# Kernel tuning notes

Measured on AMD Instinct MI355X. Metric: run time of the kernel, lower is better.

## Reference

```python
import jax, jax.numpy as jnp
import numpy as np

DIM = 2048
NH = 16
HD = DIM // NH
B = 2
S = 2048
HID = 5632  # multiple_of*ceil(int(2*4*dim/3)/multiple_of)
EPS = 1e-6


def setup_inputs() -> dict:
    key = jax.random.key(0)
    ks = jax.random.split(key, 9)
    sd = 0.02
    x = jax.random.normal(ks[0], (B, S, DIM), jnp.float32)
    wq = jax.random.normal(ks[1], (DIM, DIM), jnp.float32) * sd
    wk = jax.random.normal(ks[2], (DIM, DIM), jnp.float32) * sd
    wv = jax.random.normal(ks[3], (DIM, DIM), jnp.float32) * sd
    wo = jax.random.normal(ks[4], (DIM, DIM), jnp.float32) * sd
    w1 = jax.random.normal(ks[5], (DIM, HID), jnp.float32) * sd
    w2 = jax.random.normal(ks[6], (HID, DIM), jnp.float32) * sd
    w3 = jax.random.normal(ks[7], (DIM, HID), jnp.float32) * sd
    attn_norm_w = jnp.ones((DIM,), jnp.float32)
    ffn_norm_w = jnp.ones((DIM,), jnp.float32)
    # RoPE tables: freqs_cis = exp(i * t * theta_j), theta_j = 10000^(-2j/HD)
    inv_freq = 1.0 / (10000.0 ** (np.arange(0, HD, 2).astype(np.float32) / HD))
    t = np.arange(S, dtype=np.float32)
    ang = np.outer(t, inv_freq)  # [S, HD/2]
    freqs_cos = jnp.asarray(np.cos(ang), jnp.float32)
    freqs_sin = jnp.asarray(np.sin(ang), jnp.float32)
    # causal additive mask [1,1,S,S]
    mask = jnp.triu(jnp.full((S, S), float('-inf'), jnp.float32), k=1)[None, None]
    return dict(x=x, wq=wq, wk=wk, wv=wv, wo=wo, w1=w1, w2=w2, w3=w3,
                attn_norm_w=attn_norm_w, ffn_norm_w=ffn_norm_w,
                freqs_cos=freqs_cos, freqs_sin=freqs_sin, mask=mask)


def _rmsnorm(x, w):
    xf = x.astype(jnp.float32)
    v = jnp.mean(xf * xf, axis=-1, keepdims=True)
    return (xf * jax.lax.rsqrt(v + EPS)).astype(x.dtype) * w


def _rope(t, cos, sin):
    # t: [B,S,H,HD] -> pairs (re, im) on last dim
    tr = t.reshape(*t.shape[:-1], HD // 2, 2)
    re, im = tr[..., 0], tr[..., 1]
    c = cos[None, :, None, :]
    s = sin[None, :, None, :]
    out_re = re * c - im * s
    out_im = re * s + im * c
    return jnp.stack([out_re, out_im], axis=-1).reshape(t.shape)


def reference(x, wq, wk, wv, wo, w1, w2, w3, attn_norm_w, ffn_norm_w,
              freqs_cos, freqs_sin, mask):
    # --- attention sublayer ---
    h_in = _rmsnorm(x, attn_norm_w)
    xq = (h_in @ wq).reshape(B, S, NH, HD)
    xk = (h_in @ wk).reshape(B, S, NH, HD)
    xv = (h_in @ wv).reshape(B, S, NH, HD)
    xq = _rope(xq, freqs_cos, freqs_sin)
    xk = _rope(xk, freqs_cos, freqs_sin)
    scale = 1.0 / jnp.sqrt(jnp.float32(HD))
    scores = jnp.einsum('bqhd,bkhd->bhqk', xq, xk) * scale + mask
    probs = jax.nn.softmax(scores.astype(jnp.float32), axis=-1).astype(xq.dtype)
    attn = jnp.einsum('bhqk,bkhd->bqhd', probs, xv).reshape(B, S, DIM)
    h = x + attn @ wo
    # --- feedforward sublayer (SwiGLU) ---
    f_in = _rmsnorm(h, ffn_norm_w)
    ffn = (jax.nn.silu(f_in @ w1) * (f_in @ w3)) @ w2
    return h + ffn
```

## Files before the change

### kernel.cpp

```cpp
#include <hip/hip_runtime.h>

#define DIMQ 2048
#define NHQ  16
#define HDQ  128
#define BQ   2
#define SQ   2048
#define HIDQ 5632
#define MQ   (BQ * SQ)
#define SC_ATTN 0.08838834764831845f

using u16 = unsigned short;
using u32 = unsigned int;
typedef __attribute__((ext_vector_type(8))) short s16x8;
typedef __attribute__((ext_vector_type(4))) float f32x4;

__device__ __forceinline__ float bf2f(u16 v) {
  union { u32 u; float f; } w; w.u = ((u32)v) << 16; return w.f;
}
__device__ __forceinline__ u16 f2bf(float f) {
  union { float f; u32 u; } w; w.f = f;
  u32 r = w.u + 0x7FFFu + ((w.u >> 16) & 1u);
  return (u16)(r >> 16);
}

__device__ __forceinline__ f32x4 mfma16(s16x8 a, s16x8 b, f32x4 c) {
  return __builtin_amdgcn_mfma_f32_16x16x32_bf16(a, b, c, 0, 0, 0);
}

__device__ __forceinline__ void gl_lds16(const void* g, void* l) {
  __builtin_amdgcn_global_load_lds((const __attribute__((address_space(1))) void*)g,
                                   (__attribute__((address_space(3))) void*)l,
                                   16, 0, 0);
}

#define SBAR()                                   \
  {                                              \
    asm volatile("" ::: "memory");               \
    __builtin_amdgcn_s_barrier();                \
    asm volatile("" ::: "memory");               \
  }

__global__ __launch_bounds__(256) void transpose_cvt(const float* __restrict__ src,
                                                     u16* __restrict__ dst,
                                                     int R, int Cn) {
  __shared__ float tile[32][33];
  const int tx = threadIdx.x, ty = threadIdx.y;
  const int c0 = blockIdx.x * 32, r0 = blockIdx.y * 32;
#pragma unroll
  for (int i = 0; i < 4; ++i)
    tile[ty + i * 8][tx] = src[(size_t)(r0 + ty + i * 8) * Cn + c0 + tx];
  __syncthreads();
#pragma unroll
  for (int i = 0; i < 4; ++i)
    dst[(size_t)(c0 + ty + i * 8) * R + r0 + tx] = f2bf(tile[tx][ty + i * 8]);
}

__global__ __launch_bounds__(256) void vtrans_k(const u16* __restrict__ qkv,
                                                u16* __restrict__ vt) {
  __shared__ u16 tile[32][33];
  const int bh = blockIdx.z;
  const int b = bh >> 4, h = bh & 15;
  const int s0 = blockIdx.x * 32, d0 = blockIdx.y * 32;
  const int tx = threadIdx.x, ty = threadIdx.y;
  const u16* src = qkv + (size_t)(b * SQ) * 6144 + 4096 + h * HDQ;
#pragma unroll
  for (int i = 0; i < 4; ++i)
    tile[ty + i * 8][tx] = src[(size_t)(s0 + ty + i * 8) * 6144 + d0 + tx];
  __syncthreads();
  u16* dst = vt + (size_t)bh * HDQ * SQ;
#pragma unroll
  for (int i = 0; i < 4; ++i)
    dst[(size_t)(d0 + ty + i * 8) * SQ + s0 + tx] = tile[tx][ty + i * 8];
}

__global__ __launch_bounds__(256) void rmsnorm_k(const float* __restrict__ x,
                                                 const float* __restrict__ w,
                                                 u16* __restrict__ o) {
  const int row = blockIdx.x;
  const int t = threadIdx.x;
  const float* xr = x + (size_t)row * DIMQ;
  const float4 a = ((const float4*)xr)[t * 2];
  const float4 b = ((const float4*)xr)[t * 2 + 1];
  float ss = a.x * a.x + a.y * a.y + a.z * a.z + a.w * a.w +
             b.x * b.x + b.y * b.y + b.z * b.z + b.w * b.w;
#pragma unroll
  for (int off = 32; off > 0; off >>= 1) ss += __shfl_down(ss, off);
  __shared__ float red[4];
  if ((t & 63) == 0) red[t >> 6] = ss;
  __syncthreads();
  ss = red[0] + red[1] + red[2] + red[3];
  const float rs = rsqrtf(ss * (1.0f / (float)DIMQ) + 1e-6f);
  const float4 wa = ((const float4*)w)[t * 2];
  const float4 wb = ((const float4*)w)[t * 2 + 1];
  s16x8 ov;
  ov[0] = (short)f2bf(a.x * rs * wa.x);
  ov[1] = (short)f2bf(a.y * rs * wa.y);
  ov[2] = (short)f2bf(a.z * rs * wa.z);
  ov[3] = (short)f2bf(a.w * rs * wa.w);
  ov[4] = (short)f2bf(b.x * rs * wb.x);
  ov[5] = (short)f2bf(b.y * rs * wb.y);
  ov[6] = (short)f2bf(b.z * rs * wb.z);
  ov[7] = (short)f2bf(b.w * rs * wb.w);
  *(s16x8*)(o + (size_t)row * DIMQ + t * 8) = ov;
}

template <int OM, int BN>
__global__ __launch_bounds__(512, 1) void gemm256(const u16* __restrict__ A,
                                                  const u16* __restrict__ Bt,
                                                  u16* __restrict__ Cb,
                                                  float* __restrict__ Cf,
                                                  const float* __restrict__ resid,
                                                  int N, int K, int lda) {
  constexpr int BT = BN * 128;
  constexpr int BLB = BN / 128;
  constexpr int WNv = (BN == 256) ? 4 : 2;
  constexpr int MF = (BN == 256) ? 8 : 4;
  constexpr int MFH = MF / 2;
  __shared__ u16 lds[(65536 + 2 * BT) / 2];
  const int tid = threadIdx.x, wid = tid >> 6, lane = tid & 63;
  const int wm = wid / WNv, wn = wid % WNv;
  const int r = lane & 15, kc = lane >> 4;
  const int nbx = N / BN;
  const int nwg = nbx << 4;
  const int o = blockIdx.x;
  const int seq = (o & 7) * (nwg >> 3) + (o >> 3);
  const int by = seq & 15, bx = seq >> 4;
  const int m0 = by << 8, n0 = bx * BN;
  const int T = K >> 6;

  const u16* Ag = A + (size_t)m0 * lda;
  const u16* Bg = Bt + (size_t)n0 * K;

  const int pl = (tid * 16) ^ (((tid >> 3) & 7) << 4);
  const int prow = pl >> 7;
  const int pcol = (pl & 127) >> 1;

  const int rd0 = r * 128 + ((kc * 16) ^ ((r & 7) << 4));
  const int waveA = wm * (MF * 2048);
  const int waveB = wn * 8192;

  f32x4 acc[MF][4] = {};
  s16x8 af[MFH][2], bfL[2][2], bfH[2][2];

#define STAGE_A(G, kt, BUFB, h)                                                   \
  {                                                                               \
    _Pragma("unroll") for (int i = 0; i < 2; ++i)                                 \
        gl_lds16(G + (size_t)((h) * 128 + i * 64 + prow) * lda + (kt) * 64 + pcol,\
                 (char*)lds + (BUFB) + (h) * 16384 + i * 8192 + (wid << 10));     \
  }
#define STAGE_B(G, kt, BUFB, h)                                                   \
  {                                                                               \
    _Pragma("unroll") for (int i = 0; i < BLB; ++i)                               \
        gl_lds16(G + (size_t)((h) * (BN / 2) + i * 64 + prow) * K + (kt) * 64 + pcol, \
                 (char*)lds + (BUFB) + (h) * (BT / 2) + i * 8192 + (wid << 10));  \
  }

  STAGE_A(Ag, 0, 0, 0);
  STAGE_A(Ag, 0, 0, 1);
  STAGE_B(Bg, 0, 65536, 0);
  STAGE_B(Bg, 0, 65536, 1);
  STAGE_A(Ag, 1, 32768, 0);
  STAGE_A(Ag, 1, 32768, 1);
  asm volatile("s_waitcnt vmcnt(4)" ::: "memory");
  SBAR();

#define TILE_BODY(t, cur)                                                         \
  {                                                                               \
    const int tp1 = ((t) + 1 < T) ? (t) + 1 : T - 1;                              \
    const int tp2 = ((t) + 2 < T) ? (t) + 2 : T - 1;                              \
    const int AB = (cur)*32768;                                                   \
    const int BB = 65536 + (cur)*BT;                                              \
    const int BBn = 65536 + (1 - (cur)) * BT;                                     \
           \
    STAGE_B(Bg, tp1, BBn, 0);                                                     \
    _Pragma("unroll") for (int j = 0; j < MFH; ++j)                               \
        _Pragma("unroll") for (int ks = 0; ks < 2; ++ks)                          \
            af[j][ks] = *(const s16x8*)((const char*)lds + AB + waveA +           \
                                        j * 2048 + (rd0 ^ (ks << 6)));            \
    _Pragma("unroll") for (int n = 0; n < 2; ++n)                                 \
        _Pragma("unroll") for (int ks = 0; ks < 2; ++ks)                          \
            bfL[n][ks] = *(const s16x8*)((const char*)lds + BB + waveB +          \
                                         n * 2048 + (rd0 ^ (ks << 6)));           \
    __builtin_amdgcn_s_setprio(1);                                                \
    _Pragma("unroll") for (int ks = 0; ks < 2; ++ks)                              \
        _Pragma("unroll") for (int j = 0; j < MFH; ++j)                           \
            _Pragma("unroll") for (int n = 0; n < 2; ++n)                         \
                acc[j][n] = mfma16(af[j][ks], bfL[n][ks], acc[j][n]);             \
    __builtin_amdgcn_s_setprio(0);                                                \
                 \
    STAGE_B(Bg, tp1, BBn, 1);                                                     \
    _Pragma("unroll") for (int n = 0; n < 2; ++n)                                 \
        _Pragma("unroll") for (int ks = 0; ks < 2; ++ks)                          \
            bfH[n][ks] = *(const s16x8*)((const char*)lds + BB + waveB +          \
                                         (2 + n) * 2048 + (rd0 ^ (ks << 6)));     \
    __builtin_amdgcn_s_setprio(1);                                                \
    _Pragma("unroll") for (int ks = 0; ks < 2; ++ks)                              \
        _Pragma("unroll") for (int j = 0; j < MFH; ++j)                           \
            _Pragma("unroll") for (int n = 0; n < 2; ++n)                         \
                acc[j][2 + n] = mfma16(af[j][ks], bfH[n][ks], acc[j][2 + n]);     \
    __builtin_amdgcn_s_setprio(0);                                                \
                                  \
    _Pragma("unroll") for (int j = 0; j < MFH; ++j)                               \
        _Pragma("unroll") for (int ks = 0; ks < 2; ++ks)                          \
            af[j][ks] = *(const s16x8*)((const char*)lds + AB + waveA +           \
                                        (MFH + j) * 2048 + (rd0 ^ (ks << 6)));    \
    __builtin_amdgcn_s_setprio(1);                                                \
    _Pragma("unroll") for (int ks = 0; ks < 2; ++ks)                              \
        _Pragma("unroll") for (int j = 0; j < MFH; ++j)                           \
            _Pragma("unroll") for (int n = 0; n < 2; ++n)                         \
                acc[MFH + j][n] = mfma16(af[j][ks], bfL[n][ks], acc[MFH + j][n]); \
    __builtin_amdgcn_s_setprio(0);                                                \
    SBAR();     \
                  \
    STAGE_A(Ag, tp2, AB, 0);                                                      \
    STAGE_A(Ag, tp2, AB, 1);                                                      \
    __builtin_amdgcn_s_setprio(1);                                                \
    _Pragma("unroll") for (int ks = 0; ks < 2; ++ks)                              \
        _Pragma("unroll") for (int j = 0; j < MFH; ++j)                           \
            _Pragma("unroll") for (int n = 0; n < 2; ++n)                         \
                acc[MFH + j][2 + n] = mfma16(af[j][ks], bfH[n][ks], acc[MFH + j][2 + n]); \
    __builtin_amdgcn_s_setprio(0);                                                \
    asm volatile("s_waitcnt vmcnt(4)" ::: "memory");    \
    SBAR();                                                                       \
  }

  for (int tt = 0; tt < T; tt += 2) {
    TILE_BODY(tt, 0);
    TILE_BODY(tt + 1, 1);
  }
#undef TILE_BODY
#undef STAGE_A
#undef STAGE_B

#pragma unroll
  for (int mf = 0; mf < MF; ++mf)
#pragma unroll
    for (int nf = 0; nf < 4; ++nf)
#pragma unroll
      for (int j = 0; j < 4; ++j) {
        const int rr = m0 + wm * (MF * 16) + mf * 16 + kc * 4 + j;
        const int cc = n0 + wn * 64 + nf * 16 + r;
        const float v = acc[mf][nf][j];
        if (OM == 0) {
          Cb[(size_t)rr * N + cc] = f2bf(v);
        } else {
          Cf[(size_t)rr * N + cc] = v + resid[(size_t)rr * N + cc];
        }
      }
}

__global__ __launch_bounds__(256) void rope_k(u16* __restrict__ qkv,
                                              const float* __restrict__ fc,
                                              const float* __restrict__ fs) {
  const int row = blockIdx.x;
  const int s = row & (SQ - 1);
  const int t = threadIdx.x;
  const int p0 = t * 8;
  const int hs = p0 >> 6;
  const int i0 = p0 & 63;
  u16* base = qkv + (size_t)row * 6144 + hs * HDQ + 2 * i0;
  union { s16x8 v[2]; u16 e[16]; } d;
  d.v[0] = *(const s16x8*)base;
  d.v[1] = *(const s16x8*)(base + 8);
  const float4 c0 = *(const float4*)&fc[(size_t)s * 64 + i0];
  const float4 c1 = *(const float4*)&fc[(size_t)s * 64 + i0 + 4];
  const float4 sn0 = *(const float4*)&fs[(size_t)s * 64 + i0];
  const float4 sn1 = *(const float4*)&fs[(size_t)s * 64 + i0 + 4];
  const float cv[8] = {c0.x, c0.y, c0.z, c0.w, c1.x, c1.y, c1.z, c1.w};
  const float sv[8] = {sn0.x, sn0.y, sn0.z, sn0.w, sn1.x, sn1.y, sn1.z, sn1.w};
#pragma unroll
  for (int k = 0; k < 8; ++k) {
    const float re = bf2f(d.e[2 * k]);
    const float im = bf2f(d.e[2 * k + 1]);
    d.e[2 * k] = f2bf(re * cv[k] - im * sv[k]);
    d.e[2 * k + 1] = f2bf(re * sv[k] + im * cv[k]);
  }
  *(s16x8*)base = d.v[0];
  *(s16x8*)(base + 8) = d.v[1];
}

__global__ __launch_bounds__(256) void attn_k(const u16* __restrict__ qkv,
                                              const u16* __restrict__ vt,
                                              u16* __restrict__ outb) {
  __shared__ u16 Kl[64 * 136];
  __shared__ u16 Vl[128 * 72];
  __shared__ u16 Pl[4][16 * 80];
  const int bh = blockIdx.x;
  const int qt = 31 - blockIdx.y;
  const int b = bh >> 4, h = bh & 15;
  const int q0 = qt * 64;
  const int tid = threadIdx.x, wid = tid >> 6, lane = tid & 63;
  const int r = lane & 15, kc = lane >> 4;
  const size_t base = (size_t)b * SQ * 6144;
  const u16* vtb = vt + (size_t)bh * HDQ * SQ;
  s16x8 qf[4];
  {
    const size_t qoff = base + (size_t)(q0 + wid * 16 + r) * 6144 + h * HDQ;
#pragma unroll
    for (int kk = 0; kk < 4; ++kk)
      qf[kk] = *(const s16x8*)&qkv[qoff + kk * 32 + kc * 8];
  }
  f32x4 acc_o[8] = {};
  float m_run[4], l_run[4];
#pragma unroll
  for (int j = 0; j < 4; ++j) { m_run[j] = -1e30f; l_run[j] = 0.f; }
  const int nt = qt + 1;
  const int skey = tid >> 2, sseg = (tid & 3) * 32;
  const int vd = tid >> 1, vseg = (tid & 1) * 32;
  for (int t = 0; t < nt; ++t) {
    const int kv0 = t * 64;
    __syncthreads();
    {
      const u16* kg = &qkv[base + (size_t)(kv0 + skey) * 6144 + 2048 + h * HDQ + sseg];
      const u16* vg = &vtb[(size_t)vd * SQ + kv0 + vseg];
#pragma unroll
      for (int jj = 0; jj < 4; ++jj)
        *(s16x8*)&Kl[skey * 136 + sseg + jj * 8] = *(const s16x8*)(kg + jj * 8);
#pragma unroll
      for (int jj = 0; jj < 4; ++jj)
        *(s16x8*)&Vl[vd * 72 + vseg + jj * 8] = *(const s16x8*)(vg + jj * 8);
    }
    __syncthreads();
    f32x4 sacc[4] = {};
#pragma unroll
    for (int nf = 0; nf < 4; ++nf)
#pragma unroll
      for (int kk = 0; kk < 4; ++kk) {
        const s16x8 kf = *(const s16x8*)&Kl[(nf * 16 + r) * 136 + kk * 32 + kc * 8];
        sacc[nf] = mfma16(qf[kk], kf, sacc[nf]);
      }
    float p[4][4], alpha[4];
#pragma unroll
    for (int j = 0; j < 4; ++j) {
      const int qrow = q0 + wid * 16 + kc * 4 + j;
      float svs[4];
      float tm = -1e30f;
#pragma unroll
      for (int nf = 0; nf < 4; ++nf) {
        const int key = kv0 + nf * 16 + r;
        float sv = sacc[nf][j] * SC_ATTN;
        sv = (key > qrow) ? -1e30f : sv;
        svs[nf] = sv;
        tm = fmaxf(tm, sv);
      }
      tm = fmaxf(tm, __shfl_xor(tm, 1));
      tm = fmaxf(tm, __shfl_xor(tm, 2));
      tm = fmaxf(tm, __shfl_xor(tm, 4));
      tm = fmaxf(tm, __shfl_xor(tm, 8));
      const float mnew = fmaxf(m_run[j], tm);
      alpha[j] = __expf(m_run[j] - mnew);
      m_run[j] = mnew;
      float rs = 0.f;
#pragma unroll
      for (int nf = 0; nf < 4; ++nf) {
        const float pv = __expf(svs[nf] - mnew);
        p[nf][j] = pv;
        rs += pv;
      }
      rs += __shfl_xor(rs, 1);
      rs += __shfl_xor(rs, 2);
      rs += __shfl_xor(rs, 4);
      rs += __shfl_xor(rs, 8);
      l_run[j] = l_run[j] * alpha[j] + rs;
    }
#pragma unroll
    for (int nf = 0; nf < 8; ++nf)
#pragma unroll
      for (int j = 0; j < 4; ++j)
        acc_o[nf][j] *= alpha[j];
#pragma unroll
    for (int nf = 0; nf < 4; ++nf)
#pragma unroll
      for (int j = 0; j < 4; ++j)
        Pl[wid][(kc * 4 + j) * 80 + nf * 16 + r] = f2bf(p[nf][j]);
#pragma unroll
    for (int ks = 0; ks < 2; ++ks) {
      const s16x8 pa = *(const s16x8*)&Pl[wid][r * 80 + ks * 32 + kc * 8];
#pragma unroll
      for (int nf = 0; nf < 8; ++nf) {
        const s16x8 bv = *(const s16x8*)&Vl[(nf * 16 + r) * 72 + ks * 32 + kc * 8];
        acc_o[nf] = mfma16(pa, bv, acc_o[nf]);
      }
    }
  }
#pragma unroll
  for (int j = 0; j < 4; ++j) {
    const float inv = 1.0f / l_run[j];
    const size_t orow = (size_t)(b * SQ + q0 + wid * 16 + kc * 4 + j) * DIMQ + h * HDQ;
#pragma unroll
    for (int nf = 0; nf < 8; ++nf)
      outb[orow + nf * 16 + r] = f2bf(acc_o[nf][j] * inv);
  }
}

__global__ __launch_bounds__(64) void silu2_k(u16* __restrict__ gu) {
  const int row = blockIdx.y;
  const int c = (blockIdx.x * 64 + threadIdx.x) * 8;
  u16* gp = gu + (size_t)row * 11264 + c;
  const u16* up = gp + 5632;
  s16x8 gv = *(const s16x8*)gp;
  const s16x8 uv = *(const s16x8*)up;
#pragma unroll
  for (int e = 0; e < 8; ++e) {
    const float fg = bf2f((u16)gv[e]);
    const float fu = bf2f((u16)uv[e]);
    const float sg = fg / (1.f + __expf(-fg));
    gv[e] = (short)f2bf(sg * fu);
  }
  *(s16x8*)gp = gv;
}

extern "C" void kernel_launch(void* const* d_in, const int* in_sizes, int n_in,
                              void* d_out, int out_size, void* d_ws, size_t ws_size,
                              hipStream_t stream) {
  const float* x   = (const float*)d_in[0];
  const float* wq  = (const float*)d_in[1];
  const float* wk  = (const float*)d_in[2];
  const float* wv  = (const float*)d_in[3];
  const float* wo  = (const float*)d_in[4];
  const float* w1  = (const float*)d_in[5];
  const float* w2  = (const float*)d_in[6];
  const float* w3  = (const float*)d_in[7];
  const float* anw = (const float*)d_in[8];
  const float* fnw = (const float*)d_in[9];
  const float* fc  = (const float*)d_in[10];
  const float* fs  = (const float*)d_in[11];
  float* out = (float*)d_out;

  char* ws = (char*)d_ws;
  u16* wqkvT = (u16*)(ws);
  u16* woT   = (u16*)(ws + 25165824);
  u16* w13T  = (u16*)(ws + 25165824 + 8388608);
  u16* w2T   = (u16*)(ws + 25165824 + 8388608 + 46137344);
  u16* hin   = (u16*)(ws + 102760448);
  u16* gu    = (u16*)(ws + 119537664);
  u16* qkvb  = gu;
  u16* attnb = (u16*)(ws + 119537664 + 50331648);
  u16* vtb   = (u16*)(ws + 119537664 + 50331648 + 16777216);
  float* h = out;

  const dim3 tb(32, 8);
  transpose_cvt<<<dim3(64, 64), tb, 0, stream>>>(wq, wqkvT, 2048, 2048);
  transpose_cvt<<<dim3(64, 64), tb, 0, stream>>>(wk, wqkvT + (size_t)2048 * 2048, 2048, 2048);
  transpose_cvt<<<dim3(64, 64), tb, 0, stream>>>(wv, wqkvT + (size_t)2 * 2048 * 2048, 2048, 2048);
  transpose_cvt<<<dim3(64, 64), tb, 0, stream>>>(wo, woT, 2048, 2048);
  transpose_cvt<<<dim3(176, 64), tb, 0, stream>>>(w1, w13T, 2048, 5632);
  transpose_cvt<<<dim3(176, 64), tb, 0, stream>>>(w3, w13T + (size_t)5632 * 2048, 2048, 5632);
  transpose_cvt<<<dim3(64, 176), tb, 0, stream>>>(w2, w2T, 5632, 2048);

  rmsnorm_k<<<4096, 256, 0, stream>>>(x, anw, hin);
  gemm256<0, 128><<<768, 512, 0, stream>>>(hin, wqkvT, qkvb, nullptr, nullptr, 6144, 2048, 2048);
  rope_k<<<4096, 256, 0, stream>>>(qkvb, fc, fs);
  vtrans_k<<<dim3(64, 4, 32), tb, 0, stream>>>(qkvb, vtb);
  attn_k<<<dim3(32, 32), 256, 0, stream>>>(qkvb, vtb, attnb);
  gemm256<1, 128><<<256, 512, 0, stream>>>(attnb, woT, nullptr, h, x, 2048, 2048, 2048);
  rmsnorm_k<<<4096, 256, 0, stream>>>(h, fnw, hin);
  gemm256<0, 256><<<704, 512, 0, stream>>>(hin, w13T, gu, nullptr, nullptr, 11264, 2048, 2048);
  silu2_k<<<dim3(11, 4096), 64, 0, stream>>>(gu);
  gemm256<1, 128><<<256, 512, 0, stream>>>(gu, w2T, nullptr, out, h, 2048, 5632, 11264);
}
```

Before: 661.4 us.

## Fuse RoPE into QKV GEMM epilogue and SwiGLU into interleaved W1/W3 GEMM

Applies RoPE inside the QKV GEMM epilogue, using a lane shuffle to fetch each pair's partner value, which removes the separate rope kernel and its read/write pass over Q and K. The W1 and W3 weights are interleaved in 128-column blocks so a new gemm_ffn kernel computes the gate and up tiles in the same workgroup and writes silu(g)*u directly. This drops the silu kernel and halves the intermediate activation buffer the down-projection reads. In exchange the epilogue does scalar cos/sin table loads, and the block index mapping changes from a fixed shift to a division by the number of column blocks.

```diff
diff --git a/kernel.cpp b/kernel.cpp
--- a/kernel.cpp
+++ b/kernel.cpp
@@ -53,6 +53,24 @@
 #pragma unroll
   for (int i = 0; i < 4; ++i)
     dst[(size_t)(c0 + ty + i * 8) * R + r0 + tx] = f2bf(tile[tx][ty + i * 8]);
+}
+
+__global__ __launch_bounds__(256) void transpose_cvt_ffn(const float* __restrict__ src,
+                                                         u16* __restrict__ dst,
+                                                         int base) {
+  __shared__ float tile[32][33];
+  const int tx = threadIdx.x, ty = threadIdx.y;
+  const int c0 = blockIdx.x * 32, r0 = blockIdx.y * 32;
+#pragma unroll
+  for (int i = 0; i < 4; ++i)
+    tile[ty + i * 8][tx] = src[(size_t)(r0 + ty + i * 8) * HIDQ + c0 + tx];
+  __syncthreads();
+#pragma unroll
+  for (int i = 0; i < 4; ++i) {
+    const int n = c0 + ty + i * 8;
+    const int row = (n >> 7) * 256 + base + (n & 127);
+    dst[(size_t)row * DIMQ + r0 + tx] = f2bf(tile[tx][ty + i * 8]);
+  }
 }
 
 __global__ __launch_bounds__(256) void vtrans_k(const u16* __restrict__ qkv,
@@ -104,12 +122,14 @@
   *(s16x8*)(o + (size_t)row * DIMQ + t * 8) = ov;
 }
 
-template <int OM, int BN>
+template <int OM, int BN, int ROPE>
 __global__ __launch_bounds__(512, 1) void gemm256(const u16* __restrict__ A,
                                                   const u16* __restrict__ Bt,
                                                   u16* __restrict__ Cb,
                                                   float* __restrict__ Cf,
                                                   const float* __restrict__ resid,
+                                                  const float* __restrict__ fc,
+                                                  const float* __restrict__ fs,
                                                   int N, int K, int lda) {
   constexpr int BT = BN * 128;
   constexpr int BLB = BN / 128;
@@ -124,7 +144,7 @@
   const int nwg = nbx << 4;
   const int o = blockIdx.x;
   const int seq = (o & 7) * (nwg >> 3) + (o >> 3);
-  const int by = seq & 15, bx = seq >> 4;
+  const int by = seq / nbx, bx = seq - by * nbx;
   const int m0 = by << 8, n0 = bx * BN;
   const int T = K >> 6;
 
@@ -232,6 +252,7 @@
 #undef STAGE_A
 #undef STAGE_B
 
+  const bool do_rope = ROPE && (n0 < 4096);
 #pragma unroll
   for (int mf = 0; mf < MF; ++mf)
 #pragma unroll
@@ -240,8 +261,18 @@
       for (int j = 0; j < 4; ++j) {
         const int rr = m0 + wm * (MF * 16) + mf * 16 + kc * 4 + j;
         const int cc = n0 + wn * 64 + nf * 16 + r;
-        const float v = acc[mf][nf][j];
+        float v = acc[mf][nf][j];
         if (OM == 0) {
+          if (ROPE) {
+            const float partner = __shfl_xor(v, 1);
+            if (do_rope) {
+              const int s = rr & (SQ - 1);
+              const int i0 = (cc >> 1) & 63;
+              const float cv = fc[s * 64 + i0];
+              const float sv = fs[s * 64 + i0];
+              v = ((r & 1) == 0) ? v * cv - partner * sv : v * cv + partner * sv;
+            }
+          }
           Cb[(size_t)rr * N + cc] = f2bf(v);
         } else {
           Cf[(size_t)rr * N + cc] = v + resid[(size_t)rr * N + cc];
@@ -249,34 +280,133 @@
       }
 }
 
-__global__ __launch_bounds__(256) void rope_k(u16* __restrict__ qkv,
-                                              const float* __restrict__ fc,
-                                              const float* __restrict__ fs) {
-  const int row = blockIdx.x;
-  const int s = row & (SQ - 1);
-  const int t = threadIdx.x;
-  const int p0 = t * 8;
-  const int hs = p0 >> 6;
-  const int i0 = p0 & 63;
-  u16* base = qkv + (size_t)row * 6144 + hs * HDQ + 2 * i0;
-  union { s16x8 v[2]; u16 e[16]; } d;
-  d.v[0] = *(const s16x8*)base;
-  d.v[1] = *(const s16x8*)(base + 8);
-  const float4 c0 = *(const float4*)&fc[(size_t)s * 64 + i0];
-  const float4 c1 = *(const float4*)&fc[(size_t)s * 64 + i0 + 4];
-  const float4 sn0 = *(const float4*)&fs[(size_t)s * 64 + i0];
-  const float4 sn1 = *(const float4*)&fs[(size_t)s * 64 + i0 + 4];
-  const float cv[8] = {c0.x, c0.y, c0.z, c0.w, c1.x, c1.y, c1.z, c1.w};
-  const float sv[8] = {sn0.x, sn0.y, sn0.z, sn0.w, sn1.x, sn1.y, sn1.z, sn1.w};
-#pragma unroll
-  for (int k = 0; k < 8; ++k) {
-    const float re = bf2f(d.e[2 * k]);
-    const float im = bf2f(d.e[2 * k + 1]);
-    d.e[2 * k] = f2bf(re * cv[k] - im * sv[k]);
-    d.e[2 * k + 1] = f2bf(re * sv[k] + im * cv[k]);
-  }
-  *(s16x8*)base = d.v[0];
-  *(s16x8*)(base + 8) = d.v[1];
+__global__ __launch_bounds__(512, 1) void gemm_ffn(const u16* __restrict__ A,
+                                                   const u16* __restrict__ Bi,
+                                                   u16* __restrict__ act) {
+  __shared__ u16 lds[65536];
+  const int tid = threadIdx.x, wid = tid >> 6, lane = tid & 63;
+  const int wm = wid >> 1, wn = wid & 1;
+  const int r = lane & 15, kc = lane >> 4;
+  const int o = blockIdx.x;
+  const int seq = (o & 7) * 88 + (o >> 3);
+  const int by = seq / 44, bx = seq - by * 44;
+  const int m0 = by << 8;
+  const int T = 32;
+
+  const u16* Ag = A + (size_t)m0 * DIMQ;
+  const u16* Bg = Bi + (size_t)bx * 256 * DIMQ;
+
+  const int pl = (tid * 16) ^ (((tid >> 3) & 7) << 4);
+  const int prow = pl >> 7, pcol = (pl & 127) >> 1;
+  const int rd0 = r * 128 + ((kc * 16) ^ ((r & 7) << 4));
+  const int waveA = wm * 8192;
+  const int waveB = wn * 8192;
+
+  f32x4 accG[4][4] = {}, accU[4][4] = {};
+  s16x8 af[4][2], bL[2][2], bH[2][2];
+
+#define STG(G, kt, BUFB, h)                                                       \
+  {                                                                               \
+    _Pragma("unroll") for (int i = 0; i < 2; ++i)                                 \
+        gl_lds16(G + (size_t)((h) * 128 + i * 64 + prow) * DIMQ + (kt) * 64 + pcol,\
+                 (char*)lds + (BUFB) + (h) * 16384 + i * 8192 + (wid << 10));     \
+  }
+
+  STG(Ag, 0, 0, 0);
+  STG(Ag, 0, 0, 1);
+  STG(Bg, 0, 65536, 0);
+  STG(Bg, 0, 65536, 1);
+  STG(Ag, 1, 32768, 0);
+  STG(Ag, 1, 32768, 1);
+  asm volatile("s_waitcnt vmcnt(4)" ::: "memory");
+  SBAR();
+
+#define FFN_BODY(t, cur)                                                          \
+  {                                                                               \
+    const int tp1 = ((t) + 1 < T) ? (t) + 1 : T - 1;                              \
+    const int tp2 = ((t) + 2 < T) ? (t) + 2 : T - 1;                              \
+    const int AB = (cur)*32768;                                                   \
+    const int BB = 65536 + (cur)*32768;                                           \
+    const int BBn = 65536 + (1 - (cur)) * 32768;                                  \
+                            \
+    STG(Bg, tp1, BBn, 0);                                                         \
+    _Pragma("unroll") for (int j = 0; j < 4; ++j)                                 \
+        _Pragma("unroll") for (int ks = 0; ks < 2; ++ks)                          \
+            af[j][ks] = *(const s16x8*)((const char*)lds + AB + waveA +           \
+                                        j * 2048 + (rd0 ^ (ks << 6)));            \
+    _Pragma("unroll") for (int n = 0; n < 2; ++n)                                 \
+        _Pragma("unroll") for (int ks = 0; ks < 2; ++ks)                          \
+            bL[n][ks] = *(const s16x8*)((const char*)lds + BB + waveB +           \
+                                        n * 2048 + (rd0 ^ (ks << 6)));            \
+    __builtin_amdgcn_s_setprio(1);                                                \
+    _Pragma("unroll") for (int ks = 0; ks < 2; ++ks)                              \
+        _Pragma("unroll") for (int j = 0; j < 4; ++j)                             \
+            _Pragma("unroll") for (int n = 0; n < 2; ++n)                         \
+                accG[j][n] = mfma16(af[j][ks], bL[n][ks], accG[j][n]);            \
+    __builtin_amdgcn_s_setprio(0);                                                \
+                                 \
+    STG(Bg, tp1, BBn, 1);                                                         \
+    _Pragma("unroll") for (int n = 0; n < 2; ++n)                                 \
+        _Pragma("unroll") for (int ks = 0; ks < 2; ++ks)                          \
+            bH[n][ks] = *(const s16x8*)((const char*)lds + BB + waveB +           \
+                                        (2 + n) * 2048 + (rd0 ^ (ks << 6)));      \
+    __builtin_amdgcn_s_setprio(1);                                                \
+    _Pragma("unroll") for (int ks = 0; ks < 2; ++ks)                              \
+        _Pragma("unroll") for (int j = 0; j < 4; ++j)                             \
+            _Pragma("unroll") for (int n = 0; n < 2; ++n)                         \
+                accG[j][2 + n] = mfma16(af[j][ks], bH[n][ks], accG[j][2 + n]);    \
+    __builtin_amdgcn_s_setprio(0);                                                \
+                                                    \
+    _Pragma("unroll") for (int n = 0; n < 2; ++n)                                 \
+        _Pragma("unroll") for (int ks = 0; ks < 2; ++ks)                          \
+            bL[n][ks] = *(const s16x8*)((const char*)lds + BB + 16384 + waveB +   \
+                                        n * 2048 + (rd0 ^ (ks << 6)));            \
+    __builtin_amdgcn_s_setprio(1);                                                \
+    _Pragma("unroll") for (int ks = 0; ks < 2; ++ks)                              \
+        _Pragma("unroll") for (int j = 0; j < 4; ++j)                             \
+            _Pragma("unroll") for (int n = 0; n < 2; ++n)                         \
+                accU[j][n] = mfma16(af[j][ks], bL[n][ks], accU[j][n]);            \
+    __builtin_amdgcn_s_setprio(0);                                                \
+          \
+    _Pragma("unroll") for (int n = 0; n < 2; ++n)                                 \
+        _Pragma("unroll") for (int ks = 0; ks < 2; ++ks)                          \
+            bH[n][ks] = *(const s16x8*)((const char*)lds + BB + 16384 + waveB +   \
+                                        (2 + n) * 2048 + (rd0 ^ (ks << 6)));      \
+    SBAR();                        \
+                                                 \
+    STG(Ag, tp2, AB, 0);                                                          \
+    STG(Ag, tp2, AB, 1);                                                          \
+    __builtin_amdgcn_s_setprio(1);                                                \
+    _Pragma("unroll") for (int ks = 0; ks < 2; ++ks)                              \
+        _Pragma("unroll") for (int j = 0; j < 4; ++j)                             \
+            _Pragma("unroll") for (int n = 0; n < 2; ++n)                         \
+                accU[j][2 + n] = mfma16(af[j][ks], bH[n][ks], accU[j][2 + n]);    \
+    __builtin_amdgcn_s_setprio(0);                                                \
+    asm volatile("s_waitcnt vmcnt(4)" ::: "memory");                              \
+    SBAR();                                                                       \
+  }
+
+  for (int tt = 0; tt < T; tt += 2) {
+    FFN_BODY(tt, 0);
+    FFN_BODY(tt + 1, 1);
+  }
+#undef FFN_BODY
+#undef STG
+
+  const int cbase = bx * 128 + wn * 64;
+#pragma unroll
+  for (int mf = 0; mf < 4; ++mf)
+#pragma unroll
+    for (int nf = 0; nf < 4; ++nf)
+#pragma unroll
+      for (int j = 0; j < 4; ++j) {
+        const int rr = m0 + wm * 64 + mf * 16 + kc * 4 + j;
+        const int cc = cbase + nf * 16 + r;
+        const float g = accG[mf][nf][j];
+        const float u = accU[mf][nf][j];
+        const float a = g / (1.f + __expf(-g)) * u;
+        act[(size_t)rr * HIDQ + cc] = f2bf(a);
+      }
 }
 
 __global__ __launch_bounds__(256) void attn_k(const u16* __restrict__ qkv,
@@ -393,23 +523,6 @@
   }
 }
 
-__global__ __launch_bounds__(64) void silu2_k(u16* __restrict__ gu) {
-  const int row = blockIdx.y;
-  const int c = (blockIdx.x * 64 + threadIdx.x) * 8;
-  u16* gp = gu + (size_t)row * 11264 + c;
-  const u16* up = gp + 5632;
-  s16x8 gv = *(const s16x8*)gp;
-  const s16x8 uv = *(const s16x8*)up;
-#pragma unroll
-  for (int e = 0; e < 8; ++e) {
-    const float fg = bf2f((u16)gv[e]);
-    const float fu = bf2f((u16)uv[e]);
-    const float sg = fg / (1.f + __expf(-fg));
-    gv[e] = (short)f2bf(sg * fu);
-  }
-  *(s16x8*)gp = gv;
-}
-
 extern "C" void kernel_launch(void* const* d_in, const int* in_sizes, int n_in,
                               void* d_out, int out_size, void* d_ws, size_t ws_size,
                               hipStream_t stream) {
@@ -430,11 +543,11 @@
   char* ws = (char*)d_ws;
   u16* wqkvT = (u16*)(ws);
   u16* woT   = (u16*)(ws + 25165824);
-  u16* w13T  = (u16*)(ws + 25165824 + 8388608);
+  u16* w13i  = (u16*)(ws + 25165824 + 8388608);
   u16* w2T   = (u16*)(ws + 25165824 + 8388608 + 46137344);
   u16* hin   = (u16*)(ws + 102760448);
-  u16* gu    = (u16*)(ws + 119537664);
-  u16* qkvb  = gu;
+  u16* qkvb  = (u16*)(ws + 119537664);
+  u16* act   = qkvb;
   u16* attnb = (u16*)(ws + 119537664 + 50331648);
   u16* vtb   = (u16*)(ws + 119537664 + 50331648 + 16777216);
   float* h = out;
@@ -444,18 +557,16 @@
   transpose_cvt<<<dim3(64, 64), tb, 0, stream>>>(wk, wqkvT + (size_t)2048 * 2048, 2048, 2048);
   transpose_cvt<<<dim3(64, 64), tb, 0, stream>>>(wv, wqkvT + (size_t)2 * 2048 * 2048, 2048, 2048);
   transpose_cvt<<<dim3(64, 64), tb, 0, stream>>>(wo, woT, 2048, 2048);
-  transpose_cvt<<<dim3(176, 64), tb, 0, stream>>>(w1, w13T, 2048, 5632);
-  transpose_cvt<<<dim3(176, 64), tb, 0, stream>>>(w3, w13T + (size_t)5632 * 2048, 2048, 5632);
+  transpose_cvt_ffn<<<dim3(176, 64), tb, 0, stream>>>(w1, w13i, 0);
+  transpose_cvt_ffn<<<dim3(176, 64), tb, 0, stream>>>(w3, w13i, 128);
   transpose_cvt<<<dim3(64, 176), tb, 0, stream>>>(w2, w2T, 5632, 2048);
 
   rmsnorm_k<<<4096, 256, 0, stream>>>(x, anw, hin);
-  gemm256<0, 128><<<768, 512, 0, stream>>>(hin, wqkvT, qkvb, nullptr, nullptr, 6144, 2048, 2048);
-  rope_k<<<4096, 256, 0, stream>>>(qkvb, fc, fs);
+  gemm256<0, 128, 1><<<768, 512, 0, stream>>>(hin, wqkvT, qkvb, nullptr, nullptr, fc, fs, 6144, 2048, 2048);
   vtrans_k<<<dim3(64, 4, 32), tb, 0, stream>>>(qkvb, vtb);
   attn_k<<<dim3(32, 32), 256, 0, stream>>>(qkvb, vtb, attnb);
-  gemm256<1, 128><<<256, 512, 0, stream>>>(attnb, woT, nullptr, h, x, 2048, 2048, 2048);
+  gemm256<1, 128, 0><<<256, 512, 0, stream>>>(attnb, woT, nullptr, h, x, nullptr, nullptr, 2048, 2048, 2048);
   rmsnorm_k<<<4096, 256, 0, stream>>>(h, fnw, hin);
-  gemm256<0, 256><<<704, 512, 0, stream>>>(hin, w13T, gu, nullptr, nullptr, 11264, 2048, 2048);
-  silu2_k<<<dim3(11, 4096), 64, 0, stream>>>(gu);
-  gemm256<1, 128><<<256, 512, 0, stream>>>(gu, w2T, nullptr, out, h, 2048, 5632, 11264);
-}
+  gemm_ffn<<<704, 512, 0, stream>>>(hin, w13i, act);
+  gemm256<1, 128, 0><<<256, 512, 0, stream>>>(act, w2T, nullptr, out, h, nullptr, nullptr, 2048, 5632, 5632);
+}
```

Measured after the change: 633.1 us. -4.3%, faster.
